# Optimization experiments

Measured on AMD Instinct MI355X. Metric: run time of the kernel, lower is better.

The kernel has to match this reference:

```python
import jax, jax.numpy as jnp
import numpy as np

D_IN = 1024
D_MODEL = 1024
NUM_HEADS = 16
DEPTH = D_MODEL // NUM_HEADS


def setup_inputs() -> dict:
    key = jax.random.key(0)
    ks = jax.random.split(key, 7)
    B, N = 2, 2048
    s = 1.0 / np.sqrt(D_IN)
    return {
        "x": jax.random.normal(ks[0], (B, N, D_IN), dtype=jnp.float32),
        "Wq": jax.random.normal(ks[1], (D_IN, D_MODEL), dtype=jnp.float32) * s,
        "bq": jnp.zeros((D_MODEL,), dtype=jnp.float32),
        "Wk": jax.random.normal(ks[2], (D_IN, D_MODEL), dtype=jnp.float32) * s,
        "bk": jnp.zeros((D_MODEL,), dtype=jnp.float32),
        "Wv": jax.random.normal(ks[3], (D_IN, D_MODEL), dtype=jnp.float32) * s,
        "bv": jnp.zeros((D_MODEL,), dtype=jnp.float32),
    }


def _split_heads(t):
    B, N, _ = t.shape
    return t.reshape(B, N, NUM_HEADS, DEPTH).transpose(0, 2, 1, 3)  # [B,H,N,depth]


def reference(x, Wq, bq, Wk, bk, Wv, bv):
    B, N, _ = x.shape
    q = _split_heads(x @ Wq + bq)
    k = _split_heads(x @ Wk + bk)
    v = _split_heads(x @ Wv + bv)
    scale = 1.0 / jnp.sqrt(jnp.float32(DEPTH))
    attn = jnp.einsum("bhnd,bhmd->bhnm", q, k) * scale  # [B,H,N,N]
    attn = jax.nn.softmax(attn, axis=-1)
    out = jnp.einsum("bhnm,bhmd->bhnd", attn, v)
    return out.transpose(0, 2, 1, 3).reshape(B, N, D_MODEL)
```

## Files before the change

### kernel.cpp

```cpp
#include <hip/hip_runtime.h>
#include <cstdint>


#define SEQ_N 2048
#define NHEAD 16
#define DEPTH 64
#define SCALE_Q (0.125f * 1.44269504088896340736f)
#define M_OFF (-12.0f)

typedef short bf16x8 __attribute__((ext_vector_type(8)));
typedef short short4v __attribute__((ext_vector_type(4)));
typedef float f32x4 __attribute__((ext_vector_type(4)));

#define MFMA32(a, b, c) __builtin_amdgcn_mfma_f32_16x16x32_bf16((a), (b), (c), 0, 0, 0)

#if defined(__has_builtin)
#if __has_builtin(__builtin_amdgcn_exp2f)
#define FEXP2(x) __builtin_amdgcn_exp2f(x)
#endif
#endif
#ifndef FEXP2
#define FEXP2(x) exp2f(x)
#endif

__device__ __forceinline__ short f2b(float f) {
    union { float f; unsigned u; } v; v.f = f;
    unsigned u = v.u;
    return (short)((u + 0x7FFFu + ((u >> 16) & 1u)) >> 16);
}

__device__ __forceinline__ unsigned cvt_pk_bf16(float lo, float hi) {
    unsigned r;
    asm("v_cvt_pk_bf16_f32 %0, %1, %2" : "=v"(r) : "v"(lo), "v"(hi));
    return r;
}

__device__ __forceinline__ void gld_lds16(const void* g, void* l) {
    __builtin_amdgcn_global_load_lds(
        (const __attribute__((address_space(1))) unsigned int*)(uintptr_t)g,
        (__attribute__((address_space(3))) unsigned int*)(uintptr_t)l, 16, 0, 0);
}

__global__ __launch_bounds__(256) void cvt_all_kernel(
    const float* __restrict__ x, short* __restrict__ xb,
    const float* __restrict__ Wq, const float* __restrict__ Wk,
    const float* __restrict__ Wv, short* __restrict__ WT)
{
    __shared__ float tile[64][65];
    if (blockIdx.x < 2048) {
        const int i = blockIdx.x * 256 + threadIdx.x;
        const float4* xi = (const float4*)x + (size_t)i * 2;
        const float4 a = xi[0], c = xi[1];
        bf16x8 o;
        o[0] = f2b(a.x); o[1] = f2b(a.y); o[2] = f2b(a.z); o[3] = f2b(a.w);
        o[4] = f2b(c.x); o[5] = f2b(c.y); o[6] = f2b(c.z); o[7] = f2b(c.w);
        *((bf16x8*)xb + i) = o;
        return;
    }
    const int bid = blockIdx.x - 2048;
    const int mat = bid >> 8;
    const int t = bid & 255;
    const int k0 = (t >> 4) * 64, n0 = (t & 15) * 64;
    const float* W = (mat == 0) ? Wq : ((mat == 1) ? Wk : Wv);
    const int tt = threadIdx.x;
#pragma unroll
    for (int i = 0; i < 16; ++i) {
        const int idx = tt + i * 256;
        const int r = idx >> 6, c = idx & 63;
        tile[r][c] = W[(size_t)(k0 + r) * 1024 + n0 + c];
    }
    __syncthreads();
#pragma unroll
    for (int i = 0; i < 16; ++i) {
        const int idx = tt + i * 256;
        const int r = idx >> 6, c = idx & 63;
        WT[(size_t)(mat * 1024 + n0 + r) * 1024 + k0 + c] = f2b(tile[c][r]);
    }
}

#define GEMM_K 1024

__global__ __launch_bounds__(256) void qkv_gemm_kernel(
    const short* __restrict__ A, const short* __restrict__ BT,
    const float* __restrict__ bq, const float* __restrict__ bk, const float* __restrict__ bv,
    short* __restrict__ Qb, short* __restrict__ Kb, short* __restrict__ VTb)
{
    __shared__ short As[2][128 * 32];
    __shared__ short Bs[2][128 * 32];
    const int tid = threadIdx.x;
    const int l = tid & 63;
    const int w = tid >> 6;
    const int wr = w >> 1, wc = w & 1;
    const int bm = blockIdx.x & 31;
    const int bn = blockIdx.x >> 5;
    const int row0 = bm * 128, col0 = bn * 128;
    const int lr = l & 15, lk = l >> 4;

    const int r0 = tid >> 2;
    const int g0 = (tid & 3) ^ ((r0 >> 1) & 3);
    const int g1 = (tid & 3) ^ (((r0 + 64) >> 1) & 3);
    const int sw = (lr >> 1) & 3;
    const int aA = (wr * 64 + lr) * 32 + ((lk ^ sw) << 3);
    const int aB = (wc * 64 + lr) * 32 + ((lk ^ sw) << 3);

#define GSTAGE(BUF, KT)                                                               \
    do {                                                                              \
        gld_lds16(A + (size_t)(row0 + r0) * GEMM_K + (KT) * 32 + g0 * 8,              \
                  &As[BUF][tid * 8]);                                                 \
        gld_lds16(BT + (size_t)(col0 + r0) * GEMM_K + (KT) * 32 + g0 * 8,             \
                  &Bs[BUF][tid * 8]);                                                 \
        gld_lds16(A + (size_t)(row0 + r0 + 64) * GEMM_K + (KT) * 32 + g1 * 8,         \
                  &As[BUF][2048 + tid * 8]);                                          \
        gld_lds16(BT + (size_t)(col0 + r0 + 64) * GEMM_K + (KT) * 32 + g1 * 8,        \
                  &Bs[BUF][2048 + tid * 8]);                                          \
    } while (0)

    f32x4 acc[4][4];
#pragma unroll
    for (int m = 0; m < 4; ++m)
#pragma unroll
        for (int n = 0; n < 4; ++n) acc[m][n] = (f32x4){0.f, 0.f, 0.f, 0.f};

    GSTAGE(0, 0);
    asm volatile("s_waitcnt vmcnt(0)" ::: "memory");
    __builtin_amdgcn_s_barrier();
    __builtin_amdgcn_sched_barrier(0);

    for (int kt = 0; kt < GEMM_K / 32; ++kt) {
        const int cur = kt & 1;
        const int ktn = (kt + 1 < GEMM_K / 32) ? kt + 1 : GEMM_K / 32 - 1;
        GSTAGE(cur ^ 1, ktn);

        bf16x8 af[4], bfr[4];
#pragma unroll
        for (int m = 0; m < 4; ++m)
            af[m] = *(const bf16x8*)(&As[cur][0] + m * 512 + aA);
#pragma unroll
        for (int n = 0; n < 4; ++n)
            bfr[n] = *(const bf16x8*)(&Bs[cur][0] + n * 512 + aB);
#pragma unroll
        for (int m = 0; m < 4; ++m)
#pragma unroll
            for (int n = 0; n < 4; ++n)
                acc[m][n] = MFMA32(af[m], bfr[n], acc[m][n]);

        asm volatile("s_waitcnt vmcnt(0)" ::: "memory");
        __builtin_amdgcn_s_barrier();
        __builtin_amdgcn_sched_barrier(0);
    }
#undef GSTAGE

#pragma unroll
    for (int n = 0; n < 4; ++n) {
        const int gcol = col0 + wc * 64 + n * 16 + lr;
        const int mat = gcol >> 10;
        const int jj = gcol & 1023;
        const float bias = ((mat == 0) ? bq : ((mat == 1) ? bk : bv))[jj];
        const int h = jj >> 6, d = jj & 63;
        if (mat < 2) {
            short* O = (mat == 0) ? Qb : Kb;
            const float sc = (mat == 0) ? SCALE_Q : 1.0f;
#pragma unroll
            for (int m = 0; m < 4; ++m)
#pragma unroll
                for (int r = 0; r < 4; ++r) {
                    const int grow = row0 + wr * 64 + m * 16 + lk * 4 + r;
                    const int bb = grow >> 11, ns = grow & 2047;
                    O[(size_t)((bb * NHEAD + h) * SEQ_N + ns) * DEPTH + d] =
                        f2b((acc[m][n][r] + bias) * sc);
                }
        } else {
#pragma unroll
            for (int m = 0; m < 4; ++m) {
                const int grow0 = row0 + wr * 64 + m * 16 + lk * 4;
                const int bb = grow0 >> 11, ns0 = grow0 & 2047;
                const int g = (ns0 >> 2) & 15;
                const int gp = (g & 8) | ((g & 3) << 1) | ((g >> 2) & 1);
                const int nsp = (ns0 & ~63) | (gp << 2);
                short4v pv;
#pragma unroll
                for (int r = 0; r < 4; ++r) pv[r] = f2b(acc[m][n][r] + bias);
                *(short4v*)(VTb + ((size_t)(bb * NHEAD + h) * DEPTH + d) * SEQ_N + nsp) = pv;
            }
        }
    }
}


__device__ __forceinline__ float exppack32_lane(const f32x4 s[4], bf16x8 pb[2]) {
    float rs = 0.f;
#pragma unroll
    for (int kk = 0; kk < 2; ++kk) {
        union { unsigned u[4]; bf16x8 v; } pk;
#pragma unroll
        for (int hh = 0; hh < 2; ++hh) {
            const int c = 2 * kk + hh;
            const float p0 = FEXP2(s[c][0]);
            const float p1 = FEXP2(s[c][1]);
            const float p2 = FEXP2(s[c][2]);
            const float p3 = FEXP2(s[c][3]);
            rs += (p0 + p1) + (p2 + p3);
            pk.u[2 * hh]     = cvt_pk_bf16(p0, p1);
            pk.u[2 * hh + 1] = cvt_pk_bf16(p2, p3);
        }
        pb[kk] = pk.v;
    }
    return rs;
}

#define NT 16

__global__ __launch_bounds__(256, 2) void attn_kernel(
    const short* __restrict__ Qb, const short* __restrict__ Kb,
    const short* __restrict__ VTb, float* __restrict__ out)
{
    __shared__ short smem[2][16384];

    const int tid = threadIdx.x;
    const int l = tid & 63, w = tid >> 6;
    const int lr = l & 15, lk = l >> 4;

    const int hb = blockIdx.x;
    const int slot = hb >> 3;
    const int bh = (hb & 7) * 4 + (slot >> 4);
    const int qt = slot & 15;
    const int b = bh >> 4, h = bh & 15;

    const int qw = qt * 128 + w * 32;

    const short* Qg = Qb + ((size_t)bh * SEQ_N + qw + lr) * DEPTH + lk * 8;
    const bf16x8 bq00 = *(const bf16x8*)(Qg);
    const bf16x8 bq01 = *(const bf16x8*)(Qg + 32);
    const bf16x8 bq10 = *(const bf16x8*)(Qg + 16 * DEPTH);
    const bf16x8 bq11 = *(const bf16x8*)(Qg + 16 * DEPTH + 32);

    const short* Kg = Kb + (size_t)bh * SEQ_N * DEPTH;
    const short* Vg = VTb + (size_t)bh * DEPTH * SEQ_N;

    const int srow = tid >> 3;
    const int sg = (tid & 7) ^ (srow & 7);
    const short* Ksrc = Kg + (size_t)srow * DEPTH + sg * 8;
    const short* Vsrc = Vg + (size_t)srow * SEQ_N + sg * 8;

#define STAGE(BUF, T)                                                            \
    do {                                                                         \
        const int key0_ = (T) * 128;                                             \
        short* dst = &smem[BUF][w * 512];                                        \
        gld_lds16(Ksrc + (size_t)key0_ * DEPTH, dst);                            \
        gld_lds16(Ksrc + (size_t)(key0_ + 32) * DEPTH, dst + 2048);              \
        gld_lds16(Ksrc + (size_t)(key0_ + 64) * DEPTH, dst + 4096);              \
        gld_lds16(Ksrc + (size_t)(key0_ + 96) * DEPTH, dst + 6144);              \
        gld_lds16(Vsrc + key0_, dst + 8192);                                     \
        gld_lds16(Vsrc + key0_ + 32 * SEQ_N, dst + 10240);                       \
        gld_lds16(Vsrc + key0_ + 64, dst + 12288);                               \
        gld_lds16(Vsrc + key0_ + 64 + 32 * SEQ_N, dst + 14336);                  \
    } while (0)

    const short* s0p = &smem[0][0];
    const int aoff0 = lr * 64 + (((lk    ) ^ (lr & 7)) << 3);
    const int aoff1 = lr * 64 + (((lk + 4) ^ (lr & 7)) << 3);

    f32x4 acc0[4], acc1[4];
#pragma unroll
    for (int n = 0; n < 4; ++n) {
        acc0[n] = (f32x4){0.f, 0.f, 0.f, 0.f};
        acc1[n] = (f32x4){0.f, 0.f, 0.f, 0.f};
    }
    float l0 = 0.f, l1 = 0.f;

    STAGE(0, 0);
    asm volatile("s_waitcnt vmcnt(0)" ::: "memory");
    __builtin_amdgcn_s_barrier();
    __builtin_amdgcn_sched_barrier(0);

#pragma unroll 2
    for (int t = 0; t < NT; ++t) {
        const int cur = t & 1;
        const int tn = (t + 1 < NT) ? (t + 1) : (NT - 1);
        STAGE(cur ^ 1, tn);

#pragma unroll
        for (int ss = 0; ss < 2; ++ss) {
            const int sub = ss ^ (w & 1);
            const short* Kl = s0p + cur * 16384 + sub * 4096;
            const short* Vl = Kl + 8192;

            bf16x8 kf[4][2], vf[4][2];
#pragma unroll
            for (int c = 0; c < 4; ++c) {
                kf[c][0] = *(const bf16x8*)(Kl + c * 1024 + aoff0);
                kf[c][1] = *(const bf16x8*)(Kl + c * 1024 + aoff1);
            }
#pragma unroll
            for (int n = 0; n < 4; ++n) {
                vf[n][0] = *(const bf16x8*)(Vl + n * 1024 + aoff0);
                vf[n][1] = *(const bf16x8*)(Vl + n * 1024 + aoff1);
            }

            f32x4 s0[4], s1[4];
            __builtin_amdgcn_s_setprio(1);
#pragma unroll
            for (int c = 0; c < 4; ++c) {
                f32x4 a = (f32x4){M_OFF, M_OFF, M_OFF, M_OFF};
                a = MFMA32(kf[c][0], bq00, a);
                a = MFMA32(kf[c][1], bq01, a);
                s0[c] = a;
                f32x4 bb2 = (f32x4){M_OFF, M_OFF, M_OFF, M_OFF};
                bb2 = MFMA32(kf[c][0], bq10, bb2);
                bb2 = MFMA32(kf[c][1], bq11, bb2);
                s1[c] = bb2;
            }
            __builtin_amdgcn_s_setprio(0);

            bf16x8 pb0[2], pb1[2];
            l0 += exppack32_lane(s0, pb0);
            l1 += exppack32_lane(s1, pb1);

            __builtin_amdgcn_s_setprio(1);
#pragma unroll
            for (int n = 0; n < 4; ++n) {
                acc0[n] = MFMA32(vf[n][0], pb0[0], acc0[n]);
                acc0[n] = MFMA32(vf[n][1], pb0[1], acc0[n]);
                acc1[n] = MFMA32(vf[n][0], pb1[0], acc1[n]);
                acc1[n] = MFMA32(vf[n][1], pb1[1], acc1[n]);
            }
            __builtin_amdgcn_s_setprio(0);
        }

        asm volatile("s_waitcnt vmcnt(0)" ::: "memory");
        __builtin_amdgcn_s_barrier();
        __builtin_amdgcn_sched_barrier(0);
    }
#undef STAGE

    l0 += __shfl_xor(l0, 16); l0 += __shfl_xor(l0, 32);
    l1 += __shfl_xor(l1, 16); l1 += __shfl_xor(l1, 32);

    const float inv0 = 1.0f / l0, inv1 = 1.0f / l1;
    float* o0 = out + ((size_t)b * SEQ_N + qw + lr) * 1024 + h * 64 + lk * 4;
    float* o1 = o0 + (size_t)16 * 1024;
#pragma unroll
    for (int n = 0; n < 4; ++n) {
        const f32x4 v0 = acc0[n] * inv0;
        const f32x4 v1 = acc1[n] * inv1;
        *(f32x4*)(o0 + n * 16) = v0;
        *(f32x4*)(o1 + n * 16) = v1;
    }
}

extern "C" void kernel_launch(void* const* d_in, const int* in_sizes, int n_in,
                              void* d_out, int out_size, void* d_ws, size_t ws_size,
                              hipStream_t stream) {
    const float* x  = (const float*)d_in[0];
    const float* Wq = (const float*)d_in[1];
    const float* bq = (const float*)d_in[2];
    const float* Wk = (const float*)d_in[3];
    const float* bk = (const float*)d_in[4];
    const float* Wv = (const float*)d_in[5];
    const float* bv = (const float*)d_in[6];
    float* out = (float*)d_out;

    char* ws = (char*)d_ws;
    short* xb  = (short*)(ws);
    short* WT  = (short*)(ws + (8  << 20));
    short* Qb  = (short*)(ws + (14 << 20));
    short* Kb  = (short*)(ws + (22 << 20));
    short* VTb = (short*)(ws + (30 << 20));

    cvt_all_kernel<<<2816, 256, 0, stream>>>(x, xb, Wq, Wk, Wv, WT);
    qkv_gemm_kernel<<<32 * 24, 256, 0, stream>>>(xb, WT, bq, bk, bv, Qb, Kb, VTb);
    attn_kernel<<<512, 256, 0, stream>>>(Qb, Kb, VTb, out);
}
```

Before: 83.55 us.

## Overlap prefetch with compute via partial vmcnt waits; stage Q/K epilogue through LDS

Both the QKV GEMM and the attention loops now issue the next tile's loads and then wait only for the previous tile's loads (vmcnt(4)/vmcnt(8)) instead of draining everything after the compute. This keeps the prefetch in flight while the current tile is being computed, with a barrier at the end of each iteration to protect buffer reuse. The Q/K epilogue of the GEMM is also rewritten to stage results in padded LDS and then write full 128-byte head rows with vector stores, replacing scattered 2-byte global writes. This adds an extra barrier per iteration and relies on the vmcnt counts matching the number of loads issued per stage.

```diff
diff --git a/kernel.cpp b/kernel.cpp
--- a/kernel.cpp
+++ b/kernel.cpp
@@ -79,14 +79,14 @@
 }
 
 #define GEMM_K 1024
+#define GEMM_NK (GEMM_K / 32)
 
 __global__ __launch_bounds__(256) void qkv_gemm_kernel(
     const short* __restrict__ A, const short* __restrict__ BT,
     const float* __restrict__ bq, const float* __restrict__ bk, const float* __restrict__ bv,
     short* __restrict__ Qb, short* __restrict__ Kb, short* __restrict__ VTb)
 {
-    __shared__ short As[2][128 * 32];
-    __shared__ short Bs[2][128 * 32];
+    __shared__ __align__(16) short sm[17408];
     const int tid = threadIdx.x;
     const int l = tid & 63;
     const int w = tid >> 6;
@@ -103,16 +103,19 @@
     const int aA = (wr * 64 + lr) * 32 + ((lk ^ sw) << 3);
     const int aB = (wc * 64 + lr) * 32 + ((lk ^ sw) << 3);
 
-#define GSTAGE(BUF, KT)                                                               \
-    do {                                                                              \
-        gld_lds16(A + (size_t)(row0 + r0) * GEMM_K + (KT) * 32 + g0 * 8,              \
-                  &As[BUF][tid * 8]);                                                 \
-        gld_lds16(BT + (size_t)(col0 + r0) * GEMM_K + (KT) * 32 + g0 * 8,             \
-                  &Bs[BUF][tid * 8]);                                                 \
-        gld_lds16(A + (size_t)(row0 + r0 + 64) * GEMM_K + (KT) * 32 + g1 * 8,         \
-                  &As[BUF][2048 + tid * 8]);                                          \
-        gld_lds16(BT + (size_t)(col0 + r0 + 64) * GEMM_K + (KT) * 32 + g1 * 8,        \
-                  &Bs[BUF][2048 + tid * 8]);                                          \
+    const short* As0 = A + (size_t)(row0 + r0) * GEMM_K + g0 * 8;
+    const short* As1 = A + (size_t)(row0 + r0 + 64) * GEMM_K + g1 * 8;
+    const short* Bs0 = BT + (size_t)(col0 + r0) * GEMM_K + g0 * 8;
+    const short* Bs1 = BT + (size_t)(col0 + r0 + 64) * GEMM_K + g1 * 8;
+
+#define GSTAGE(BUF, KT)                                            \
+    do {                                                           \
+        short* asb = sm + (BUF) * 4096;                            \
+        short* bsb = sm + 8192 + (BUF) * 4096;                     \
+        gld_lds16(As0 + (KT) * 32, &asb[tid * 8]);                 \
+        gld_lds16(Bs0 + (KT) * 32, &bsb[tid * 8]);                 \
+        gld_lds16(As1 + (KT) * 32, &asb[2048 + tid * 8]);          \
+        gld_lds16(Bs1 + (KT) * 32, &bsb[2048 + tid * 8]);          \
     } while (0)
 
     f32x4 acc[4][4];
@@ -122,54 +125,72 @@
         for (int n = 0; n < 4; ++n) acc[m][n] = (f32x4){0.f, 0.f, 0.f, 0.f};
 
     GSTAGE(0, 0);
-    asm volatile("s_waitcnt vmcnt(0)" ::: "memory");
-    __builtin_amdgcn_s_barrier();
-    __builtin_amdgcn_sched_barrier(0);
-
-    for (int kt = 0; kt < GEMM_K / 32; ++kt) {
+
+#pragma unroll 2
+    for (int kt = 0; kt < GEMM_NK; ++kt) {
         const int cur = kt & 1;
-        const int ktn = (kt + 1 < GEMM_K / 32) ? kt + 1 : GEMM_K / 32 - 1;
-        GSTAGE(cur ^ 1, ktn);
-
+        if (kt + 1 < GEMM_NK) {
+            GSTAGE(cur ^ 1, kt + 1);
+            asm volatile("s_waitcnt vmcnt(4)" ::: "memory");
+        } else {
+            asm volatile("s_waitcnt vmcnt(0)" ::: "memory");
+        }
+        __builtin_amdgcn_s_barrier();
+        __builtin_amdgcn_sched_barrier(0);
+
+        const short* asb = sm + cur * 4096;
+        const short* bsb = sm + 8192 + cur * 4096;
         bf16x8 af[4], bfr[4];
 #pragma unroll
         for (int m = 0; m < 4; ++m)
-            af[m] = *(const bf16x8*)(&As[cur][0] + m * 512 + aA);
+            af[m] = *(const bf16x8*)(asb + m * 512 + aA);
 #pragma unroll
         for (int n = 0; n < 4; ++n)
-            bfr[n] = *(const bf16x8*)(&Bs[cur][0] + n * 512 + aB);
+            bfr[n] = *(const bf16x8*)(bsb + n * 512 + aB);
 #pragma unroll
         for (int m = 0; m < 4; ++m)
 #pragma unroll
             for (int n = 0; n < 4; ++n)
                 acc[m][n] = MFMA32(af[m], bfr[n], acc[m][n]);
 
-        asm volatile("s_waitcnt vmcnt(0)" ::: "memory");
-        __builtin_amdgcn_s_barrier();
         __builtin_amdgcn_sched_barrier(0);
+        __builtin_amdgcn_s_barrier();
     }
 #undef GSTAGE
 
-#pragma unroll
-    for (int n = 0; n < 4; ++n) {
-        const int gcol = col0 + wc * 64 + n * 16 + lr;
-        const int mat = gcol >> 10;
-        const int jj = gcol & 1023;
-        const float bias = ((mat == 0) ? bq : ((mat == 1) ? bk : bv))[jj];
-        const int h = jj >> 6, d = jj & 63;
-        if (mat < 2) {
-            short* O = (mat == 0) ? Qb : Kb;
-            const float sc = (mat == 0) ? SCALE_Q : 1.0f;
-#pragma unroll
-            for (int m = 0; m < 4; ++m)
-#pragma unroll
-                for (int r = 0; r < 4; ++r) {
-                    const int grow = row0 + wr * 64 + m * 16 + lk * 4 + r;
-                    const int bb = grow >> 11, ns = grow & 2047;
-                    O[(size_t)((bb * NHEAD + h) * SEQ_N + ns) * DEPTH + d] =
-                        f2b((acc[m][n][r] + bias) * sc);
-                }
-        } else {
+    const int matb = bn >> 3;
+    if (matb < 2) {
+        short* Ct = sm;
+        short* O = (matb == 0) ? Qb : Kb;
+        const float sc = (matb == 0) ? SCALE_Q : 1.0f;
+        const float* bias = (matb == 0) ? bq : bk;
+#pragma unroll
+        for (int n = 0; n < 4; ++n) {
+            const int lc = wc * 64 + n * 16 + lr;
+            const float bb_ = bias[(col0 + lc) & 1023];
+#pragma unroll
+            for (int m = 0; m < 4; ++m) {
+                const int lrow = wr * 64 + m * 16 + lk * 4;
+#pragma unroll
+                for (int r = 0; r < 4; ++r)
+                    Ct[(lrow + r) * 136 + lc] = f2b((acc[m][n][r] + bb_) * sc);
+            }
+        }
+        __builtin_amdgcn_s_barrier();
+        const int row = tid >> 1, seg = tid & 1;
+        const int h = ((col0 + seg * 64) & 1023) >> 6;
+        const int grow = row0 + row;
+        const int bb2 = grow >> 11, ns = grow & 2047;
+        const int4* src = (const int4*)(Ct + row * 136 + seg * 64);
+        int4* dst = (int4*)(O + (size_t)((bb2 * NHEAD + h) * SEQ_N + ns) * DEPTH);
+#pragma unroll
+        for (int i = 0; i < 8; ++i) dst[i] = src[i];
+    } else {
+#pragma unroll
+        for (int n = 0; n < 4; ++n) {
+            const int jj = (col0 + wc * 64 + n * 16 + lr) & 1023;
+            const float bias = bv[jj];
+            const int h = jj >> 6, d = jj & 63;
 #pragma unroll
             for (int m = 0; m < 4; ++m) {
                 const int grow0 = row0 + wr * 64 + m * 16 + lk * 4;
@@ -269,15 +290,18 @@
     float l0 = 0.f, l1 = 0.f;
 
     STAGE(0, 0);
-    asm volatile("s_waitcnt vmcnt(0)" ::: "memory");
-    __builtin_amdgcn_s_barrier();
-    __builtin_amdgcn_sched_barrier(0);
 
 #pragma unroll 2
     for (int t = 0; t < NT; ++t) {
         const int cur = t & 1;
-        const int tn = (t + 1 < NT) ? (t + 1) : (NT - 1);
-        STAGE(cur ^ 1, tn);
+        if (t + 1 < NT) {
+            STAGE(cur ^ 1, t + 1);
+            asm volatile("s_waitcnt vmcnt(8)" ::: "memory");
+        } else {
+            asm volatile("s_waitcnt vmcnt(0)" ::: "memory");
+        }
+        __builtin_amdgcn_s_barrier();
+        __builtin_amdgcn_sched_barrier(0);
 
 #pragma unroll
         for (int ss = 0; ss < 2; ++ss) {
@@ -327,9 +351,8 @@
             __builtin_amdgcn_s_setprio(0);
         }
 
-        asm volatile("s_waitcnt vmcnt(0)" ::: "memory");
-        __builtin_amdgcn_s_barrier();
         __builtin_amdgcn_sched_barrier(0);
+        __builtin_amdgcn_s_barrier();
     }
 #undef STAGE
 
```

New measurement: 86.22 us. 1.03x slower.

## Restructure QKV GEMM into 256x192 tiles with phased K=64 pipeline and LDS epilogue

Applied to the files above, without the earlier changes.

Rewrites the QKV projection GEMM to use 512-thread blocks computing 256x192 output tiles with K-steps of 64, double-buffered in a single 112KB LDS array. Global-to-LDS loads for the next stage are interleaved across four MFMA phases, with setprio to favour compute, and the block IDs are remapped so that 256 blocks cover the 4096x3072 output. Q/K results are staged through LDS so they can be written as coalesced 16-byte rows. The larger tiles raise data reuse but cut the grid to one wave of 256 blocks and use much more LDS and registers per block.

```diff
diff --git a/kernel.cpp b/kernel.cpp
--- a/kernel.cpp
+++ b/kernel.cpp
@@ -78,101 +78,144 @@
     }
 }
 
-#define GEMM_K 1024
-
-__global__ __launch_bounds__(256) void qkv_gemm_kernel(
+__global__ __launch_bounds__(512, 2) void qkv_gemm_kernel(
     const short* __restrict__ A, const short* __restrict__ BT,
     const float* __restrict__ bq, const float* __restrict__ bk, const float* __restrict__ bv,
     short* __restrict__ Qb, short* __restrict__ Kb, short* __restrict__ VTb)
 {
-    __shared__ short As[2][128 * 32];
-    __shared__ short Bs[2][128 * 32];
+    __shared__ __align__(16) short sm[57344];
     const int tid = threadIdx.x;
-    const int l = tid & 63;
-    const int w = tid >> 6;
-    const int wr = w >> 1, wc = w & 1;
-    const int bm = blockIdx.x & 31;
-    const int bn = blockIdx.x >> 5;
-    const int row0 = bm * 128, col0 = bn * 128;
+    const int l = tid & 63, w = tid >> 6;
     const int lr = l & 15, lk = l >> 4;
-
-    const int r0 = tid >> 2;
-    const int g0 = (tid & 3) ^ ((r0 >> 1) & 3);
-    const int g1 = (tid & 3) ^ (((r0 + 64) >> 1) & 3);
-    const int sw = (lr >> 1) & 3;
-    const int aA = (wr * 64 + lr) * 32 + ((lk ^ sw) << 3);
-    const int aB = (wc * 64 + lr) * 32 + ((lk ^ sw) << 3);
-
-#define GSTAGE(BUF, KT)                                                               \
-    do {                                                                              \
-        gld_lds16(A + (size_t)(row0 + r0) * GEMM_K + (KT) * 32 + g0 * 8,              \
-                  &As[BUF][tid * 8]);                                                 \
-        gld_lds16(BT + (size_t)(col0 + r0) * GEMM_K + (KT) * 32 + g0 * 8,             \
-                  &Bs[BUF][tid * 8]);                                                 \
-        gld_lds16(A + (size_t)(row0 + r0 + 64) * GEMM_K + (KT) * 32 + g1 * 8,         \
-                  &As[BUF][2048 + tid * 8]);                                          \
-        gld_lds16(BT + (size_t)(col0 + r0 + 64) * GEMM_K + (KT) * 32 + g1 * 8,        \
-                  &Bs[BUF][2048 + tid * 8]);                                          \
+    const int wr = w >> 2, wcn = w & 3;
+
+    const int id2 = (blockIdx.x & 7) * 32 + (blockIdx.x >> 3);
+    const int bm = id2 & 15, bn = id2 >> 4;
+    const int row0 = bm * 256, col0 = bn * 192;
+
+    const int gsrc8 = ((tid & 7) ^ ((tid >> 3) & 7)) << 3;
+    const short* a_src = A + (size_t)(row0 + (tid >> 3)) * 1024 + gsrc8;
+    const short* b_src = BT + (size_t)(col0 + (tid >> 3)) * 1024 + gsrc8;
+
+    const int aBase = (wr * 128 + lr) * 64;
+    const int bBase = (wcn * 48 + lr) * 64;
+    const int asw0 = ((lk)     ^ (lr & 7)) << 3;
+    const int asw1 = ((lk + 4) ^ (lr & 7)) << 3;
+
+    f32x4 acc[8][3];
+#pragma unroll
+    for (int m = 0; m < 8; ++m)
+#pragma unroll
+        for (int n = 0; n < 3; ++n) acc[m][n] = (f32x4){0.f, 0.f, 0.f, 0.f};
+
+    gld_lds16(a_src,          sm + tid * 8);
+    gld_lds16(a_src + 65536,  sm + tid * 8 + 4096);
+    gld_lds16(a_src + 131072, sm + tid * 8 + 8192);
+    gld_lds16(a_src + 196608, sm + tid * 8 + 12288);
+    gld_lds16(b_src,          sm + 32768 + tid * 8);
+    gld_lds16(b_src + 65536,  sm + 32768 + tid * 8 + 4096);
+    gld_lds16(b_src + 131072, sm + 32768 + tid * 8 + 8192);
+
+#define PHASE(P, GLDS)                                                          \
+    do {                                                                        \
+        bf16x8 af[2][2];                                                        \
+        af[0][0] = *(const bf16x8*)(Al + aBase + (2*(P))*1024 + asw0);          \
+        af[0][1] = *(const bf16x8*)(Al + aBase + (2*(P))*1024 + asw1);          \
+        af[1][0] = *(const bf16x8*)(Al + aBase + (2*(P)+1)*1024 + asw0);        \
+        af[1][1] = *(const bf16x8*)(Al + aBase + (2*(P)+1)*1024 + asw1);        \
+        GLDS;                                                                   \
+        __builtin_amdgcn_s_barrier();                                           \
+        asm volatile("s_waitcnt lgkmcnt(0)" ::: "memory");                      \
+        __builtin_amdgcn_sched_barrier(0);                                      \
+        __builtin_amdgcn_s_setprio(1);                                          \
+        _Pragma("unroll")                                                       \
+        for (int mm = 0; mm < 2; ++mm)                                          \
+            _Pragma("unroll")                                                   \
+            for (int n = 0; n < 3; ++n) {                                       \
+                acc[2*(P)+mm][n] = MFMA32(af[mm][0], bfv[n][0], acc[2*(P)+mm][n]); \
+                acc[2*(P)+mm][n] = MFMA32(af[mm][1], bfv[n][1], acc[2*(P)+mm][n]); \
+            }                                                                   \
+        __builtin_amdgcn_s_setprio(0);                                          \
+        __builtin_amdgcn_s_barrier();                                           \
     } while (0)
 
-    f32x4 acc[4][4];
-#pragma unroll
-    for (int m = 0; m < 4; ++m)
-#pragma unroll
-        for (int n = 0; n < 4; ++n) acc[m][n] = (f32x4){0.f, 0.f, 0.f, 0.f};
-
-    GSTAGE(0, 0);
-    asm volatile("s_waitcnt vmcnt(0)" ::: "memory");
-    __builtin_amdgcn_s_barrier();
-    __builtin_amdgcn_sched_barrier(0);
-
-    for (int kt = 0; kt < GEMM_K / 32; ++kt) {
-        const int cur = kt & 1;
-        const int ktn = (kt + 1 < GEMM_K / 32) ? kt + 1 : GEMM_K / 32 - 1;
-        GSTAGE(cur ^ 1, ktn);
-
-        bf16x8 af[4], bfr[4];
-#pragma unroll
-        for (int m = 0; m < 4; ++m)
-            af[m] = *(const bf16x8*)(&As[cur][0] + m * 512 + aA);
-#pragma unroll
-        for (int n = 0; n < 4; ++n)
-            bfr[n] = *(const bf16x8*)(&Bs[cur][0] + n * 512 + aB);
-#pragma unroll
-        for (int m = 0; m < 4; ++m)
-#pragma unroll
-            for (int n = 0; n < 4; ++n)
-                acc[m][n] = MFMA32(af[m], bfr[n], acc[m][n]);
-
-        asm volatile("s_waitcnt vmcnt(0)" ::: "memory");
+#pragma unroll 2
+    for (int kt = 0; kt < 16; ++kt) {
+        const int cur = kt & 1, nxt = cur ^ 1;
+        const short* Al = sm + cur * 16384;
+        const short* Bl = sm + 32768 + cur * 12288;
+        short* And = sm + nxt * 16384;
+        short* Bnd = sm + 32768 + nxt * 12288;
+        const int k1 = (kt + 1) * 64;
+        const bool more = (kt < 15);
+
+        bf16x8 bfv[3][2];
+
+        if (more) {
+            gld_lds16(a_src + k1,         And + tid * 8);
+            gld_lds16(a_src + k1 + 65536, And + tid * 8 + 4096);
+            asm volatile("s_waitcnt vmcnt(2)" ::: "memory");
+        } else {
+            asm volatile("s_waitcnt vmcnt(0)" ::: "memory");
+        }
         __builtin_amdgcn_s_barrier();
         __builtin_amdgcn_sched_barrier(0);
-    }
-#undef GSTAGE
-
-#pragma unroll
-    for (int n = 0; n < 4; ++n) {
-        const int gcol = col0 + wc * 64 + n * 16 + lr;
-        const int mat = gcol >> 10;
-        const int jj = gcol & 1023;
-        const float bias = ((mat == 0) ? bq : ((mat == 1) ? bk : bv))[jj];
-        const int h = jj >> 6, d = jj & 63;
+        {
+            bf16x8 af[2][2];
+            af[0][0] = *(const bf16x8*)(Al + aBase + asw0);
+            af[0][1] = *(const bf16x8*)(Al + aBase + asw1);
+            af[1][0] = *(const bf16x8*)(Al + aBase + 1024 + asw0);
+            af[1][1] = *(const bf16x8*)(Al + aBase + 1024 + asw1);
+#pragma unroll
+            for (int n = 0; n < 3; ++n) {
+                bfv[n][0] = *(const bf16x8*)(Bl + bBase + n * 1024 + asw0);
+                bfv[n][1] = *(const bf16x8*)(Bl + bBase + n * 1024 + asw1);
+            }
+            asm volatile("s_waitcnt lgkmcnt(0)" ::: "memory");
+            __builtin_amdgcn_sched_barrier(0);
+            __builtin_amdgcn_s_setprio(1);
+#pragma unroll
+            for (int mm = 0; mm < 2; ++mm)
+#pragma unroll
+                for (int n = 0; n < 3; ++n) {
+                    acc[mm][n] = MFMA32(af[mm][0], bfv[n][0], acc[mm][n]);
+                    acc[mm][n] = MFMA32(af[mm][1], bfv[n][1], acc[mm][n]);
+                }
+            __builtin_amdgcn_s_setprio(0);
+        }
+        __builtin_amdgcn_s_barrier();
+
+        PHASE(1, if (more) { gld_lds16(a_src + k1 + 131072, And + tid * 8 + 8192);
+                             gld_lds16(a_src + k1 + 196608, And + tid * 8 + 12288); });
+        PHASE(2, if (more) { gld_lds16(b_src + k1,          Bnd + tid * 8);
+                             gld_lds16(b_src + k1 + 65536,  Bnd + tid * 8 + 4096); });
+        PHASE(3, if (more) { gld_lds16(b_src + k1 + 131072, Bnd + tid * 8 + 8192); });
+    }
+#undef PHASE
+
+    short* Cl = sm;
+#pragma unroll
+    for (int n = 0; n < 3; ++n) {
+        const int gb = col0 + wcn * 48 + n * 16;
+        const int mat = gb >> 10;
+        const int jj = (gb + lr) & 1023;
         if (mat < 2) {
-            short* O = (mat == 0) ? Qb : Kb;
+            const float bias = ((mat == 0) ? bq : bk)[jj];
             const float sc = (mat == 0) ? SCALE_Q : 1.0f;
-#pragma unroll
-            for (int m = 0; m < 4; ++m)
-#pragma unroll
-                for (int r = 0; r < 4; ++r) {
-                    const int grow = row0 + wr * 64 + m * 16 + lk * 4 + r;
-                    const int bb = grow >> 11, ns = grow & 2047;
-                    O[(size_t)((bb * NHEAD + h) * SEQ_N + ns) * DEPTH + d] =
-                        f2b((acc[m][n][r] + bias) * sc);
-                }
+            const int cc = wcn * 48 + n * 16 + lr;
+#pragma unroll
+            for (int m = 0; m < 8; ++m) {
+                const int rbase = wr * 128 + m * 16 + lk * 4;
+#pragma unroll
+                for (int r = 0; r < 4; ++r)
+                    Cl[(rbase + r) * 200 + cc] = f2b((acc[m][n][r] + bias) * sc);
+            }
         } else {
-#pragma unroll
-            for (int m = 0; m < 4; ++m) {
-                const int grow0 = row0 + wr * 64 + m * 16 + lk * 4;
+            const float bias = bv[jj];
+            const int h = jj >> 6, d = jj & 63;
+#pragma unroll
+            for (int m = 0; m < 8; ++m) {
+                const int grow0 = row0 + wr * 128 + m * 16 + lk * 4;
                 const int bb = grow0 >> 11, ns0 = grow0 & 2047;
                 const int g = (ns0 >> 2) & 15;
                 const int gp = (g & 8) | ((g & 3) << 1) | ((g >> 2) & 1);
@@ -181,6 +224,24 @@
 #pragma unroll
                 for (int r = 0; r < 4; ++r) pv[r] = f2b(acc[m][n][r] + bias);
                 *(short4v*)(VTb + ((size_t)(bb * NHEAD + h) * DEPTH + d) * SEQ_N + nsp) = pv;
+            }
+        }
+    }
+    __syncthreads();
+    {
+        const int row = tid >> 1, half = tid & 1;
+        const int grow = row0 + row;
+        const int bb = grow >> 11, ns = grow & 2047;
+#pragma unroll
+        for (int i = 0; i < 12; ++i) {
+            const int cc = half * 96 + i * 8;
+            const int gc = col0 + cc;
+            const int mat = gc >> 10;
+            if (mat < 2) {
+                short* O = mat ? Kb : Qb;
+                const int h = (gc & 1023) >> 6, d0 = gc & 63;
+                *(bf16x8*)(O + ((size_t)(bb * NHEAD + h) * SEQ_N + ns) * DEPTH + d0) =
+                    *(const bf16x8*)(Cl + row * 200 + cc);
             }
         }
     }
@@ -368,6 +429,6 @@
     short* VTb = (short*)(ws + (30 << 20));
 
     cvt_all_kernel<<<2816, 256, 0, stream>>>(x, xb, Wq, Wk, Wv, WT);
-    qkv_gemm_kernel<<<32 * 24, 256, 0, stream>>>(xb, WT, bq, bk, bv, Qb, Kb, VTb);
+    qkv_gemm_kernel<<<256, 512, 0, stream>>>(xb, WT, bq, bk, bv, Qb, Kb, VTb);
     attn_kernel<<<512, 256, 0, stream>>>(Qb, Kb, VTb, out);
 }
```

Measured after the change: 82.49 us. No clear change (-1.3%).
